# Kernel tuning notes

Measured on AMD Instinct MI355X. Metric: run time of the kernel, lower is better.

Reference implementation:

```python
import math
import jax, jax.numpy as jnp
import numpy as np

B, T, D = 2, 2048, 2048
H = 16
HD = D // H  # 128


def setup_inputs() -> dict:
    key = jax.random.key(0)
    k1, k2, k3 = jax.random.split(key, 3)
    x = jax.random.normal(k1, (B, T, D), dtype=jnp.float32)
    # Linear weights stored as [in, out] for x @ W (torch Linear weight is [out,in])
    w_attn = jax.random.normal(k2, (D, 3 * D), dtype=jnp.float32) * (1.0 / math.sqrt(D))
    w_proj = jax.random.normal(k3, (D, D), dtype=jnp.float32) * (1.0 / math.sqrt(D))
    return {"x": x, "w_attn": w_attn, "w_proj": w_proj}


def reference(x, w_attn, w_proj):
    Bc, Tc, Dc = x.shape
    qkv = x @ w_attn  # [B, T, 3D]
    q, k, v = jnp.split(qkv, 3, axis=2)
    # [B, H, T, HD]
    q = q.reshape(Bc, Tc, H, HD).transpose(0, 2, 1, 3)
    k = k.reshape(Bc, Tc, H, HD).transpose(0, 2, 1, 3)
    v = v.reshape(Bc, Tc, H, HD).transpose(0, 2, 1, 3)
    att = jnp.einsum('bhqd,bhkd->bhqk', q, k) * (1.0 / math.sqrt(HD))
    causal = jnp.tril(jnp.ones((Tc, Tc), dtype=bool))
    att = jnp.where(causal[None, None], att, -jnp.inf)
    att = jax.nn.softmax(att, axis=-1)
    y = jnp.einsum('bhqk,bhkd->bhqd', att, v)
    y = y.transpose(0, 2, 1, 3).reshape(Bc, Tc, Dc)
    return y @ w_proj
```

## Files before the change

kernel.cpp:

```cpp
#include <hip/hip_runtime.h>
#include <hip/hip_bf16.h>

#define B_ 2
#define T_ 2048
#define D_ 2048
#define H_ 16
#define HD_ 128
#define N3_ (3 * D_)
#define M_ (B_ * T_)

typedef __attribute__((ext_vector_type(8))) short short8;
typedef __attribute__((ext_vector_type(4))) short short4v;
typedef __attribute__((ext_vector_type(4))) float floatx4;

__device__ __forceinline__ ushort f2bf(float f) {
  unsigned int x = __float_as_uint(f);
  unsigned int r = (x + 0x7fffu + ((x >> 16) & 1u)) >> 16;
  return (ushort)r;
}

__device__ __forceinline__ void gload_lds16(const ushort* g, ushort* l) {
  __builtin_amdgcn_global_load_lds(
      (const __attribute__((address_space(1))) void*)g,
      (__attribute__((address_space(3))) void*)l, 16, 0, 0);
}

#define CONVB 4096
#define WATB 12288
#define WPTB 4096
__global__ __launch_bounds__(256) void prep(const float* __restrict__ x,
                                            const float* __restrict__ wa,
                                            const float* __restrict__ wp,
                                            ushort* __restrict__ xb,
                                            ushort* __restrict__ wt_attn,
                                            ushort* __restrict__ wt_proj) {
  __shared__ ushort tile[32][33];
  int bid = blockIdx.x;
  if (bid < CONVB) {
    int i = bid * 2048 + threadIdx.x * 8;
    union { ushort u[8]; short8 v; } t;
#pragma unroll
    for (int j = 0; j < 8; j++) t.u[j] = f2bf(x[i + j]);
    *(short8*)(xb + i) = t.v;
    return;
  }
  const float* in;
  ushort* out;
  int N, bx, by;
  if (bid < CONVB + WATB) {
    int id = bid - CONVB;
    N = N3_; bx = id % 192; by = id / 192; in = wa; out = wt_attn;
  } else {
    int id = bid - (CONVB + WATB);
    N = D_; bx = id & 63; by = id >> 6; in = wp; out = wt_proj;
  }
  int n0 = bx * 32, k0 = by * 32;
  int tx = threadIdx.x & 31, ty = threadIdx.x >> 5;
#pragma unroll
  for (int i = ty; i < 32; i += 8)
    tile[i][tx] = f2bf(in[(size_t)(k0 + i) * N + n0 + tx]);
  __syncthreads();
#pragma unroll
  for (int i = ty; i < 32; i += 8)
    out[(size_t)(n0 + i) * 2048 + k0 + tx] = tile[tx][i];
}

__device__ __forceinline__ void gemm128_core(const ushort* __restrict__ Ab,
                                             const ushort* __restrict__ Bb,
                                             ushort* As, ushort* Bs,
                                             floatx4 (&acc)[4][4]) {
  const int K = 2048;
  int tid = threadIdx.x, lane = tid & 63, wave = tid >> 6;
  int l16 = lane & 15, quad = lane >> 4;
  int srow = wave * 16 + (lane >> 2);
  int skq = (lane & 3) * 8;
  const ushort* ag = Ab + (size_t)srow * K + skq;
  const ushort* bg = Bb + (size_t)srow * K + skq;
  ushort* asl = As + wave * 512;
  ushort* bsl = Bs + wave * 512;
  int wr = wave >> 1, wc = wave & 1;
  const int aoff = (wr * 64 + l16) * 32 + quad * 8;
  const int boff = (wc * 64 + l16) * 32 + quad * 8;

  for (int k0 = 0; k0 < K; k0 += 32) {
    __syncthreads();
    gload_lds16(ag + k0, asl);
    gload_lds16(ag + (size_t)64 * K + k0, asl + 2048);
    gload_lds16(bg + k0, bsl);
    gload_lds16(bg + (size_t)64 * K + k0, bsl + 2048);
    __syncthreads();
    short8 af[4], bf[4];
#pragma unroll
    for (int mi = 0; mi < 4; mi++)
      af[mi] = *(const short8*)(As + aoff + mi * 512);
#pragma unroll
    for (int nj = 0; nj < 4; nj++)
      bf[nj] = *(const short8*)(Bs + boff + nj * 512);
#pragma unroll
    for (int mi = 0; mi < 4; mi++)
#pragma unroll
      for (int nj = 0; nj < 4; nj++)
        acc[mi][nj] = __builtin_amdgcn_mfma_f32_16x16x32_bf16(
            af[mi], bf[nj], acc[mi][nj], 0, 0, 0);
  }
}

__global__ __launch_bounds__(256) void gemm_qkv(const ushort* __restrict__ X,
                                                const ushort* __restrict__ Wt,
                                                ushort* __restrict__ qb,
                                                ushort* __restrict__ kb,
                                                ushort* __restrict__ vst) {
  __shared__ ushort As[4096], Bs[4096];
  floatx4 acc[4][4];
#pragma unroll
  for (int i = 0; i < 4; i++)
#pragma unroll
    for (int j = 0; j < 4; j++) acc[i][j] = (floatx4){0.f, 0.f, 0.f, 0.f};

  int m0 = blockIdx.y * 128, n0 = blockIdx.x * 128;
  gemm128_core(X + (size_t)m0 * 2048, Wt + (size_t)n0 * 2048, As, Bs, acc);

  int lane = threadIdx.x & 63, wave = threadIdx.x >> 6;
  int l16 = lane & 15, quad = lane >> 4, wr = wave >> 1, wc = wave & 1;
  int region = n0 >> 11;
  int h = (n0 & 2047) >> 7;
  int b = m0 >> 11, tb = m0 & 2047;
  if (region == 0) {
    ushort* P = qb + ((size_t)(b * H_ + h) * T_ + tb) * HD_;
#pragma unroll
    for (int mi = 0; mi < 4; mi++)
#pragma unroll
      for (int nj = 0; nj < 4; nj++)
#pragma unroll
        for (int r = 0; r < 4; r++)
          P[(size_t)(wr * 64 + mi * 16 + quad * 4 + r) * HD_ + wc * 64 +
            nj * 16 + l16] = f2bf(acc[mi][nj][r]);
  } else if (region == 1) {
    ushort* base = kb + (size_t)(b * H_ + h) * T_ * HD_;
#pragma unroll
    for (int mi = 0; mi < 4; mi++)
#pragma unroll
      for (int nj = 0; nj < 4; nj++) {
        int d = wc * 64 + nj * 16 + l16;
        int dhi = d >> 5, dlo = d & 31;
#pragma unroll
        for (int r = 0; r < 4; r++) {
          int t = tb + wr * 64 + mi * 16 + quad * 4 + r;
          base[(size_t)(t >> 6) * 8192 + dhi * 2048 + (t & 63) * 32 + dlo] =
              f2bf(acc[mi][nj][r]);
        }
      }
  } else {
    ushort* base = vst + (size_t)(b * H_ + h) * T_ * HD_;
#pragma unroll
    for (int mi = 0; mi < 4; mi++)
#pragma unroll
      for (int r = 0; r < 4; r++) {
        int t = tb + wr * 64 + mi * 16 + quad * 4 + r;
        int c = t & 63;
        int p = (c & 15) * 4 + (c >> 4);
        size_t rowbase = (size_t)(t >> 6) * 8192 + (p >> 5) * 4096 + (p & 31);
#pragma unroll
        for (int nj = 0; nj < 4; nj++) {
          int d = wc * 64 + nj * 16 + l16;
          base[rowbase + d * 32] = f2bf(acc[mi][nj][r]);
        }
      }
  }
}

__global__ __launch_bounds__(256) void gemm_proj(const ushort* __restrict__ Y,
                                                 const ushort* __restrict__ Wt,
                                                 float* __restrict__ out) {
  __shared__ ushort As[4096], Bs[4096];
  floatx4 acc[4][4];
#pragma unroll
  for (int i = 0; i < 4; i++)
#pragma unroll
    for (int j = 0; j < 4; j++) acc[i][j] = (floatx4){0.f, 0.f, 0.f, 0.f};

  int m0 = blockIdx.y * 128, n0 = blockIdx.x * 128;
  gemm128_core(Y + (size_t)m0 * 2048, Wt + (size_t)n0 * 2048, As, Bs, acc);

  int lane = threadIdx.x & 63, wave = threadIdx.x >> 6;
  int l16 = lane & 15, quad = lane >> 4, wr = wave >> 1, wc = wave & 1;
#pragma unroll
  for (int mi = 0; mi < 4; mi++)
#pragma unroll
    for (int nj = 0; nj < 4; nj++)
#pragma unroll
      for (int r = 0; r < 4; r++)
        out[(size_t)(m0 + wr * 64 + mi * 16 + quad * 4 + r) * D_ + n0 +
            wc * 64 + nj * 16 + l16] = acc[mi][nj][r];
}

__global__ __launch_bounds__(256) void attn128(const ushort* __restrict__ qb,
                                               const ushort* __restrict__ kst,
                                               const ushort* __restrict__ vst,
                                               ushort* __restrict__ y) {
  __shared__ ushort Ks[8192];
  __shared__ ushort Vs[8192];
  __shared__ ushort Ps[8192];
  int bid = blockIdx.x;
  int bh = bid & 31;
  int qt = (bid < 256) ? (bid >> 5) : (15 - ((bid - 256) >> 5));
  int q0 = qt * 128;
  int tid = threadIdx.x, lane = tid & 63, wave = tid >> 6;
  int l16 = lane & 15, quad = lane >> 4;
  int b = bh >> 4, h = bh & 15;
  const ushort* Q = qb + (size_t)bh * T_ * HD_;
  const ushort* Kt = kst + (size_t)bh * T_ * HD_;
  const ushort* Vt = vst + (size_t)bh * T_ * HD_;
  int qw0 = q0 + wave * 32;

  short8 qf[2][4];
#pragma unroll
  for (int mi = 0; mi < 2; mi++)
#pragma unroll
    for (int kk = 0; kk < 4; kk++)
      qf[mi][kk] = *(const short8*)(Q + (size_t)(qw0 + mi * 16 + l16) * HD_ +
                                    kk * 32 + quad * 8);

  floatx4 o[2][8];
#pragma unroll
  for (int mi = 0; mi < 2; mi++)
#pragma unroll
    for (int nt = 0; nt < 8; nt++) o[mi][nt] = (floatx4){0.f, 0.f, 0.f, 0.f};
  float lrow[2][4];
#pragma unroll
  for (int mi = 0; mi < 2; mi++)
#pragma unroll
    for (int r = 0; r < 4; r++) lrow[mi][r] = 0.f;

  const float scale2 = 0.08838834764831845f * 1.4426950408889634f;
  int ktiles = (q0 >> 6) + 2;

  for (int tile = 0; tile < ktiles; tile++) {
    int kt = tile << 6;
    __syncthreads();
#pragma unroll
    for (int i = 0; i < 4; i++) {
      int g = i * 256 + wave * 64;
      gload_lds16(Kt + (size_t)tile * 8192 + (g + lane) * 8, Ks + g * 8);
      gload_lds16(Vt + (size_t)tile * 8192 + (g + lane) * 8, Vs + g * 8);
    }
    __syncthreads();
    if (kt <= qw0 + 31) {
      floatx4 s[2][4];
#pragma unroll
      for (int mi = 0; mi < 2; mi++)
#pragma unroll
        for (int ng = 0; ng < 4; ng++) s[mi][ng] = (floatx4){0.f, 0.f, 0.f, 0.f};
#pragma unroll
      for (int kk = 0; kk < 4; kk++) {
        short8 kf[4];
#pragma unroll
        for (int ng = 0; ng < 4; ng++)
          kf[ng] = *(const short8*)(Ks + kk * 2048 + (ng * 16 + l16) * 32 +
                                    quad * 8);
#pragma unroll
        for (int mi = 0; mi < 2; mi++)
#pragma unroll
          for (int ng = 0; ng < 4; ng++)
            s[mi][ng] = __builtin_amdgcn_mfma_f32_16x16x32_bf16(
                qf[mi][kk], kf[ng], s[mi][ng], 0, 0, 0);
      }
      if (kt + 63 > qw0) {
#pragma unroll
        for (int mi = 0; mi < 2; mi++)
#pragma unroll
          for (int ng = 0; ng < 4; ng++)
#pragma unroll
            for (int r = 0; r < 4; r++) {
              int key = kt + ng * 16 + l16;
              int qr = qw0 + mi * 16 + quad * 4 + r;
              float p =
                  (key <= qr) ? exp2f(s[mi][ng][r] * scale2) : 0.f;
              s[mi][ng][r] = p;
              lrow[mi][r] += p;
            }
      } else {
#pragma unroll
        for (int mi = 0; mi < 2; mi++)
#pragma unroll
          for (int ng = 0; ng < 4; ng++)
#pragma unroll
            for (int r = 0; r < 4; r++) {
              float p = exp2f(s[mi][ng][r] * scale2);
              s[mi][ng][r] = p;
              lrow[mi][r] += p;
            }
      }
      ushort* Pw = Ps + wave * 2048;
#pragma unroll
      for (int mi = 0; mi < 2; mi++)
#pragma unroll
        for (int r = 0; r < 4; r++) {
          int row = mi * 16 + quad * 4 + r;
          short4v pk;
#pragma unroll
          for (int ng = 0; ng < 4; ng++) pk[ng] = (short)f2bf(s[mi][ng][r]);
          *(short4v*)(Pw + row * 64 + (((l16 >> 1) ^ (row & 7)) << 3) +
                      ((l16 & 1) << 2)) = pk;
        }
      short8 pf[2][2];
#pragma unroll
      for (int mi = 0; mi < 2; mi++)
#pragma unroll
        for (int kc = 0; kc < 2; kc++) {
          int row = mi * 16 + l16;
          pf[mi][kc] = *(const short8*)(
              Pw + row * 64 + ((((kc << 2) + quad) ^ (row & 7)) << 3));
        }
#pragma unroll
      for (int kc = 0; kc < 2; kc++)
#pragma unroll
        for (int nt = 0; nt < 8; nt++) {
          short8 vf = *(const short8*)(Vs + kc * 4096 + (nt * 16 + l16) * 32 +
                                       quad * 8);
#pragma unroll
          for (int mi = 0; mi < 2; mi++)
            o[mi][nt] = __builtin_amdgcn_mfma_f32_16x16x32_bf16(
                pf[mi][kc], vf, o[mi][nt], 0, 0, 0);
        }
    }
  }

#pragma unroll
  for (int off = 1; off < 16; off <<= 1)
#pragma unroll
    for (int mi = 0; mi < 2; mi++)
#pragma unroll
      for (int r = 0; r < 4; r++)
        lrow[mi][r] += __shfl_xor(lrow[mi][r], off);

#pragma unroll
  for (int mi = 0; mi < 2; mi++)
#pragma unroll
    for (int r = 0; r < 4; r++) {
      float inv = 1.f / lrow[mi][r];
      int t = qw0 + mi * 16 + quad * 4 + r;
#pragma unroll
      for (int nt = 0; nt < 8; nt++)
        y[((size_t)(b * T_ + t)) * D_ + h * HD_ + nt * 16 + l16] =
            f2bf(o[mi][nt][r] * inv);
    }
}

extern "C" void kernel_launch(void* const* d_in, const int* in_sizes, int n_in,
                              void* d_out, int out_size, void* d_ws,
                              size_t ws_size, hipStream_t stream) {
  const float* x = (const float*)d_in[0];
  const float* w_attn = (const float*)d_in[1];
  const float* w_proj = (const float*)d_in[2];
  float* out = (float*)d_out;

  char* ws = (char*)d_ws;
  ushort* wt_attn = (ushort*)(ws);
  ushort* wt_proj = (ushort*)(ws + 25165824);
  ushort* qb = (ushort*)(ws + 33554432);
  ushort* kb = (ushort*)(ws + 50331648);
  ushort* vst = (ushort*)(ws + 67108864);
  ushort* xb = (ushort*)(ws + 83886080);
  ushort* yb = xb;
  (void)in_sizes; (void)n_in; (void)out_size; (void)ws_size;

  prep<<<CONVB + WATB + WPTB, 256, 0, stream>>>(x, w_attn, w_proj, xb,
                                                wt_attn, wt_proj);
  gemm_qkv<<<dim3(N3_ / 128, M_ / 128), 256, 0, stream>>>(xb, wt_attn, qb, kb,
                                                          vst);
  attn128<<<B_ * H_ * (T_ / 128), 256, 0, stream>>>(qb, kb, vst, yb);
  gemm_proj<<<dim3(D_ / 128, M_ / 128), 256, 0, stream>>>(yb, wt_proj, out);
}
```

Baseline: 408.0 us.

## Double-buffer K/V tiles in attention and stage QKV epilogue through LDS

The attention kernel now keeps two K/V shared-memory buffers. It prefetches the next 64-key tile while the current one is computed, which drops one barrier per iteration and hides global-load latency. The QKV GEMM epilogue now writes the bf16 outputs into a shared staging buffer in the destination layout for Q, K or V, then copies them out with coalesced 16-byte stores instead of scattered 2-byte global writes. Both changes use more LDS (80KB in attention, 32KB in the GEMM), which may lower the number of resident blocks per CU.

Result: slower. 418.2 us (+2.5%).

```diff
diff --git a/kernel.cpp b/kernel.cpp
--- a/kernel.cpp
+++ b/kernel.cpp
@@ -110,7 +110,9 @@
                                                 ushort* __restrict__ qb,
                                                 ushort* __restrict__ kb,
                                                 ushort* __restrict__ vst) {
-  __shared__ ushort As[4096], Bs[4096];
+  __shared__ ushort Sh[16384];
+  ushort* As = Sh;
+  ushort* Bs = Sh + 4096;
   floatx4 acc[4][4];
 #pragma unroll
   for (int i = 0; i < 4; i++)
@@ -120,52 +122,40 @@
   int m0 = blockIdx.y * 128, n0 = blockIdx.x * 128;
   gemm128_core(X + (size_t)m0 * 2048, Wt + (size_t)n0 * 2048, As, Bs, acc);
 
-  int lane = threadIdx.x & 63, wave = threadIdx.x >> 6;
+  int tid = threadIdx.x, lane = tid & 63, wave = tid >> 6;
   int l16 = lane & 15, quad = lane >> 4, wr = wave >> 1, wc = wave & 1;
   int region = n0 >> 11;
   int h = (n0 & 2047) >> 7;
   int b = m0 >> 11, tb = m0 & 2047;
-  if (region == 0) {
-    ushort* P = qb + ((size_t)(b * H_ + h) * T_ + tb) * HD_;
-#pragma unroll
-    for (int mi = 0; mi < 4; mi++)
-#pragma unroll
-      for (int nj = 0; nj < 4; nj++)
-#pragma unroll
-        for (int r = 0; r < 4; r++)
-          P[(size_t)(wr * 64 + mi * 16 + quad * 4 + r) * HD_ + wc * 64 +
-            nj * 16 + l16] = f2bf(acc[mi][nj][r]);
-  } else if (region == 1) {
-    ushort* base = kb + (size_t)(b * H_ + h) * T_ * HD_;
-#pragma unroll
-    for (int mi = 0; mi < 4; mi++)
+
+  __syncthreads();
+#pragma unroll
+  for (int mi = 0; mi < 4; mi++)
+#pragma unroll
+    for (int r = 0; r < 4; r++) {
+      int tl = wr * 64 + mi * 16 + quad * 4 + r;
+      int c = tl & 63;
+      int p = (c & 15) * 4 + (c >> 4);
 #pragma unroll
       for (int nj = 0; nj < 4; nj++) {
         int d = wc * 64 + nj * 16 + l16;
-        int dhi = d >> 5, dlo = d & 31;
-#pragma unroll
-        for (int r = 0; r < 4; r++) {
-          int t = tb + wr * 64 + mi * 16 + quad * 4 + r;
-          base[(size_t)(t >> 6) * 8192 + dhi * 2048 + (t & 63) * 32 + dlo] =
-              f2bf(acc[mi][nj][r]);
-        }
+        int idx;
+        if (region == 0)
+          idx = tl * 128 + d;
+        else if (region == 1)
+          idx = (tl >> 6) * 8192 + (d >> 5) * 2048 + c * 32 + (d & 31);
+        else
+          idx = (tl >> 6) * 8192 + (p >> 5) * 4096 + d * 32 + (p & 31);
+        Sh[idx] = f2bf(acc[mi][nj][r]);
       }
-  } else {
-    ushort* base = vst + (size_t)(b * H_ + h) * T_ * HD_;
-#pragma unroll
-    for (int mi = 0; mi < 4; mi++)
-#pragma unroll
-      for (int r = 0; r < 4; r++) {
-        int t = tb + wr * 64 + mi * 16 + quad * 4 + r;
-        int c = t & 63;
-        int p = (c & 15) * 4 + (c >> 4);
-        size_t rowbase = (size_t)(t >> 6) * 8192 + (p >> 5) * 4096 + (p & 31);
-#pragma unroll
-        for (int nj = 0; nj < 4; nj++) {
-          int d = wc * 64 + nj * 16 + l16;
-          base[rowbase + d * 32] = f2bf(acc[mi][nj][r]);
-        }
-      }
+    }
+  __syncthreads();
+  ushort* dst = (region == 0 ? qb : region == 1 ? kb : vst) +
+                (size_t)(b * H_ + h) * T_ * HD_ + (size_t)tb * HD_;
+#pragma unroll
+  for (int j = 0; j < 8; j++) {
+    int off = j * 2048 + tid * 8;
+    *(short8*)(dst + off) = *(const short8*)(Sh + off);
   }
 }
 
@@ -198,8 +188,8 @@
                                                const ushort* __restrict__ kst,
                                                const ushort* __restrict__ vst,
                                                ushort* __restrict__ y) {
-  __shared__ ushort Ks[8192];
-  __shared__ ushort Vs[8192];
+  __shared__ ushort Ks[2][8192];
+  __shared__ ushort Vs[2][8192];
   __shared__ ushort Ps[8192];
   int bid = blockIdx.x;
   int bh = bid & 31;
@@ -233,18 +223,29 @@
     for (int r = 0; r < 4; r++) lrow[mi][r] = 0.f;
 
   const float scale2 = 0.08838834764831845f * 1.4426950408889634f;
-  int ktiles = (q0 >> 6) + 2;
+  int ktiles = 2 * qt + 2;
+
+#pragma unroll
+  for (int i = 0; i < 4; i++) {
+    int g = i * 256 + wave * 64;
+    gload_lds16(Kt + (size_t)(g + lane) * 8, &Ks[0][g * 8]);
+    gload_lds16(Vt + (size_t)(g + lane) * 8, &Vs[0][g * 8]);
+  }
 
   for (int tile = 0; tile < ktiles; tile++) {
     int kt = tile << 6;
+    int bsel = tile & 1;
     __syncthreads();
-#pragma unroll
-    for (int i = 0; i < 4; i++) {
-      int g = i * 256 + wave * 64;
-      gload_lds16(Kt + (size_t)tile * 8192 + (g + lane) * 8, Ks + g * 8);
-      gload_lds16(Vt + (size_t)tile * 8192 + (g + lane) * 8, Vs + g * 8);
+    if (tile + 1 < ktiles) {
+#pragma unroll
+      for (int i = 0; i < 4; i++) {
+        int g = i * 256 + wave * 64;
+        gload_lds16(Kt + (size_t)(tile + 1) * 8192 + (size_t)(g + lane) * 8,
+                    &Ks[bsel ^ 1][g * 8]);
+        gload_lds16(Vt + (size_t)(tile + 1) * 8192 + (size_t)(g + lane) * 8,
+                    &Vs[bsel ^ 1][g * 8]);
+      }
     }
-    __syncthreads();
     if (kt <= qw0 + 31) {
       floatx4 s[2][4];
 #pragma unroll
@@ -256,8 +257,8 @@
         short8 kf[4];
 #pragma unroll
         for (int ng = 0; ng < 4; ng++)
-          kf[ng] = *(const short8*)(Ks + kk * 2048 + (ng * 16 + l16) * 32 +
-                                    quad * 8);
+          kf[ng] = *(const short8*)(&Ks[bsel][kk * 2048 + (ng * 16 + l16) * 32 +
+                                             quad * 8]);
 #pragma unroll
         for (int mi = 0; mi < 2; mi++)
 #pragma unroll
@@ -274,8 +275,7 @@
             for (int r = 0; r < 4; r++) {
               int key = kt + ng * 16 + l16;
               int qr = qw0 + mi * 16 + quad * 4 + r;
-              float p =
-                  (key <= qr) ? exp2f(s[mi][ng][r] * scale2) : 0.f;
+              float p = (key <= qr) ? exp2f(s[mi][ng][r] * scale2) : 0.f;
               s[mi][ng][r] = p;
               lrow[mi][r] += p;
             }
@@ -316,8 +316,8 @@
       for (int kc = 0; kc < 2; kc++)
 #pragma unroll
         for (int nt = 0; nt < 8; nt++) {
-          short8 vf = *(const short8*)(Vs + kc * 4096 + (nt * 16 + l16) * 32 +
-                                       quad * 8);
+          short8 vf = *(const short8*)(&Vs[bsel][kc * 4096 +
+                                               (nt * 16 + l16) * 32 + quad * 8]);
 #pragma unroll
           for (int mi = 0; mi < 2; mi++)
             o[mi][nt] = __builtin_amdgcn_mfma_f32_16x16x32_bf16(
```
